# Optimization experiments

Measured on AMD Instinct MI355X. Metric: run time of the kernel, lower is better.

Reference implementation:

```python
import jax, jax.numpy as jnp
import numpy as np

NS = 33  # segments per image: id 0 = background, 1..32 = objects (fixed max-object count)
EPS_GN = 1e-5


def conv2d(x, w, b, pad):
    y = jax.lax.conv_general_dilated(x, w, window_strides=(1, 1),
                                     padding=[(pad, pad), (pad, pad)],
                                     dimension_numbers=('NCHW', 'OIHW', 'NCHW'))
    return y + b[None, :, None, None]


def group_norm(x, gamma, beta, groups):
    B, C, H, W = x.shape
    xg = x.reshape(B, groups, C // groups, H, W)
    mu = xg.mean((2, 3, 4), keepdims=True)
    var = xg.var((2, 3, 4), keepdims=True)
    xn = ((xg - mu) / jnp.sqrt(var + EPS_GN)).reshape(B, C, H, W)
    return xn * gamma[None, :, None, None] + beta[None, :, None, None]


def setup_inputs() -> dict:
    key = jax.random.key(0)
    ks = jax.random.split(key, 10)
    B, Cf, H, W = 4, 512, 128, 128
    std = 0.01
    inp = {
        'x': jax.random.normal(ks[0], (B, Cf, H, W), jnp.float32),
        'masks': jax.random.randint(ks[1], (B, H, W), 0, NS).astype(jnp.int32),
        # coord_conv: Conv2d(2, 64, 1)
        'w_coord': jax.random.normal(ks[2], (64, 2, 1, 1), jnp.float32) * std,
        'b_coord': jnp.zeros((64,), jnp.float32),
        # encoder convs + groupnorms
        'w1': jax.random.normal(ks[3], (256, Cf + 64, 3, 3), jnp.float32) * std,
        'b1': jnp.zeros((256,), jnp.float32),
        'g1': jnp.ones((256,), jnp.float32), 'bt1': jnp.zeros((256,), jnp.float32),
        'w2': jax.random.normal(ks[4], (128, 256, 3, 3), jnp.float32) * std,
        'b2': jnp.zeros((128,), jnp.float32),
        'g2': jnp.ones((128,), jnp.float32), 'bt2': jnp.zeros((128,), jnp.float32),
        'w3': jax.random.normal(ks[5], (64, 128, 3, 3), jnp.float32) * std,
        'b3': jnp.zeros((64,), jnp.float32),
        'g3': jnp.ones((64,), jnp.float32), 'bt3': jnp.zeros((64,), jnp.float32),
        # heads (1x1 convs on pooled [64] vectors == tiny matmuls)
        'w_box': jax.random.normal(ks[6], (7, 64, 1, 1), jnp.float32) * std,
        'b_box': jnp.zeros((7,), jnp.float32),
        'w_conf': jax.random.normal(ks[7], (1, 64, 1, 1), jnp.float32) * std,
        'b_conf': jnp.zeros((1,), jnp.float32),
    }
    return inp


def reference(x, masks, w_coord, b_coord, w1, b1, g1, bt1, w2, b2, g2, bt2,
              w3, b3, g3, bt3, w_box, b_box, w_conf, b_conf):
    B, _, H, W = x.shape
    # coordinate grid: channels are [grid_x, grid_y]
    gy, gx = jnp.meshgrid(jnp.arange(H), jnp.arange(W), indexing='ij')
    grid = jnp.stack([gx, gy], axis=0).astype(x.dtype)            # [2,H,W]
    grid = jnp.broadcast_to(grid[None], (B, 2, H, W))
    grid_feats = jax.nn.relu(conv2d(grid, w_coord, b_coord, 0))   # [B,64,H,W]

    h = jnp.concatenate([x, grid_feats], axis=1)                  # [B,576,H,W]
    h = jax.nn.relu(group_norm(conv2d(h, w1, b1, 1), g1, bt1, 8))
    h = jax.nn.relu(group_norm(conv2d(h, w2, b2, 1), g2, bt2, 4))
    h = jax.nn.relu(group_norm(conv2d(h, w3, b3, 1), g3, bt3, 4))  # [B,64,H,W]

    # per-(image, object-id) masked mean pooling via segment_sum
    C = h.shape[1]
    flat = h.transpose(0, 2, 3, 1).reshape(-1, C)                 # [B*H*W, 64]
    seg = (jnp.arange(B, dtype=jnp.int32)[:, None] * NS
           + masks.reshape(B, -1)).reshape(-1)                    # [B*H*W]
    sums = jax.ops.segment_sum(flat, seg, num_segments=B * NS).reshape(B, NS, C)
    counts = jax.ops.segment_sum(jnp.ones_like(seg, jnp.float32), seg,
                                 num_segments=B * NS).reshape(B, NS, 1)
    # drop background segment 0; safe divide matches the <1e-4 skip (empty slots -> 0 pooled)
    pooled = sums[:, 1:] / jnp.maximum(counts[:, 1:], 1e-4)       # [B,32,64]

    boxes = jnp.einsum('boc,kc->bok', pooled, w_box.reshape(7, C)) + b_box   # [B,32,7]
    scores = jnp.einsum('boc,c->bo', pooled, w_conf.reshape(C)) + b_conf[0]  # [B,32]
    return boxes, scores
```

## Files before the change

### kernel.cpp

```cpp
#include <hip/hip_runtime.h>

typedef unsigned short u16;
typedef unsigned int u32;
typedef __bf16 bf16x8 __attribute__((ext_vector_type(8)));
typedef float f32x4 __attribute__((ext_vector_type(4)));

__device__ __forceinline__ u16 f2bf(float f) {
  u32 u = __float_as_uint(f);
  u += 0x7fffu + ((u >> 16) & 1u);
  return (u16)(u >> 16);
}
__device__ __forceinline__ float bf2f(u16 h) {
  return __uint_as_float(((u32)h) << 16);
}

#define GLD_LDS16(g, l)                                                        \
  __builtin_amdgcn_global_load_lds(                                            \
      (__attribute__((address_space(1))) void*)(g),                            \
      (__attribute__((address_space(3))) void*)(l), 16, 0, 0)

__global__ __launch_bounds__(256) void init_k(float* smallb, u16* in1, u16* in2,
                                              u16* in3) {
  int bid = blockIdx.x;
  if (bid < 35) {
    int i = bid * 256 + threadIdx.x;
    if (i < 8708) smallb[i] = 0.f;
    return;
  }
  u16* buf;
  int C, sub;
  if (bid < 51)      { buf = in1; C = 576; sub = bid - 35; }
  else if (bid < 67) { buf = in2; C = 256; sub = bid - 51; }
  else               { buf = in3; C = 128; sub = bid - 67; }
  int b = sub >> 2, s = sub & 3;
  int npx = (s < 2) ? 130 : 128;
  u32* base = (u32*)(buf + (size_t)b * 130 * 130 * C);
  int C2 = C >> 1;
  int total = npx * C2;
  for (int i = threadIdx.x; i < total; i += 256) {
    int p = i / C2, r = i - p * C2;
    int y, x;
    if (s == 0)      { y = 0;     x = p; }
    else if (s == 1) { y = 129;   x = p; }
    else if (s == 2) { y = p + 1; x = 0; }
    else             { y = p + 1; x = 129; }
    base[(y * 130 + x) * C2 + r] = 0u;
  }
}

__global__ __launch_bounds__(256) void repack_all(const float* __restrict__ w1,
                                                  u16* __restrict__ wp1,
                                                  const float* __restrict__ w2,
                                                  u16* __restrict__ wp2,
                                                  const float* __restrict__ w3,
                                                  u16* __restrict__ wp3) {
  int bid = blockIdx.x;
  const float* src;
  u16* dst;
  int CIN, COUT, total, base;
  if (bid < 5184)      { src = w1; dst = wp1; CIN = 576; COUT = 256; total = 1327104; base = bid; }
  else if (bid < 6336) { src = w2; dst = wp2; CIN = 256; COUT = 128; total = 294912;  base = bid - 5184; }
  else                 { src = w3; dst = wp3; CIN = 128; COUT = 64;  total = 73728;   base = bid - 6336; }
  int idx = base * 256 + threadIdx.x;
  if (idx >= total) return;
  int kc = idx & 31;
  int n = (idx >> 5) % COUT;
  int q = idx / (32 * COUT);
  int dydx = q % 9, cb = q / 9;
  dst[idx] = f2bf(src[((size_t)n * CIN + cb * 32 + kc) * 9 + dydx]);
}

__global__ __launch_bounds__(256) void transpose_x(const float* __restrict__ x,
                                                   const float* __restrict__ wcd,
                                                   const float* __restrict__ bcd,
                                                   u16* __restrict__ in1) {
  const int bid = blockIdx.x;
  const int b = bid >> 8, h = (bid >> 1) & 127, half = bid & 1;
  const int w0 = half * 64;
  const int t = threadIdx.x;
  __shared__ u16 tile[128 * 65];
  __shared__ float swc[128], sbc[64];
  if (t < 128) swc[t] = wcd[t];
  else if (t < 192) sbc[t - 128] = bcd[t - 128];
  const int w = t & 63;
  const int cg = t >> 6;
  const float* xb = x + (((size_t)b * 512) * 128 + h) * 128 + w0 + w;
  u16* ob = in1 + ((size_t)(b * 130 + h + 1) * 130 + (w0 + 1)) * 576;
#pragma unroll 1
  for (int cc = 0; cc < 4; ++cc) {
    const int c0 = cc * 128;
#pragma unroll
    for (int j = 0; j < 32; ++j) {
      int cl = j * 4 + cg;
      tile[cl * 65 + w] = f2bf(xb[(size_t)(c0 + cl) * 16384]);
    }
    __syncthreads();
#pragma unroll
    for (int k = 0; k < 4; ++k) {
      int idx = k * 256 + t;
      int ww = idx >> 4, c8 = (idx & 15) * 8;
      union { uint4 u; u16 s[8]; } o;
#pragma unroll
      for (int i = 0; i < 8; ++i) o.s[i] = tile[(c8 + i) * 65 + ww];
      *(uint4*)(ob + (size_t)ww * 576 + c0 + c8) = o.u;
    }
    __syncthreads();
  }
  const int px = t >> 2, cq = (t & 3) * 16;
  const float fw = (float)(w0 + px), fh = (float)h;
  u16* gp = ob + (size_t)px * 576 + 512 + cq;
#pragma unroll
  for (int j = 0; j < 2; ++j) {
    union { uint4 u; u16 s[8]; } o;
#pragma unroll
    for (int i = 0; i < 8; ++i) {
      int c = cq + j * 8 + i;
      float v = swc[2 * c] * fw + swc[2 * c + 1] * fh + sbc[c];
      o.s[i] = f2bf(fmaxf(v, 0.f));
    }
    *(uint4*)(gp + j * 8) = o.u;
  }
}

template <int CIN, int COUT, int BN>
__global__ __launch_bounds__(256) void conv3x3_k(const u16* __restrict__ in,
                                                 const u16* __restrict__ wp,
                                                 const float* __restrict__ bias,
                                                 u16* __restrict__ out, int Hp,
                                                 int Wp, int opy, int opx,
                                                 float* __restrict__ stats,
                                                 int gsLog2, int nG) {
  constexpr int CB = CIN / 32;
  constexpr int WN = BN / 2;
  constexpr int NT = WN / 16;
  constexpr int ROWCH = 520;
  constexpr int NCH = 3 * ROWCH;
  constexpr int BUFE = 3 * 130 * 32;
  static_assert(BN == 128 || BN == 64, "");
  __shared__ u16 As3[2 * BUFE];
  __shared__ float redS[8], redQ[8];

  const int t = threadIdx.x;
  const int L = gridDim.x;
  const int work = (blockIdx.x & 7) * (L >> 3) + (blockIdx.x >> 3);
  const int xt = work >> 9;
  const int rem = work & 511;
  const int b = rem >> 7, h = rem & 127;
  const int n0 = xt * BN;

  const int lane = t & 63, wv = t >> 6;
  const int wm = wv & 1, wn = wv >> 1;
  const int ln = lane & 15, lq = lane >> 4;

  if (t < 8) { redS[t] = 0.f; redQ[t] = 0.f; }

  f32x4 acc[4][NT];
  const f32x4 zero = {0.f, 0.f, 0.f, 0.f};
#pragma unroll
  for (int i = 0; i < 4; ++i)
#pragma unroll
    for (int j = 0; j < NT; ++j) acc[i][j] = zero;

  const u16* inb = in + ((size_t)b * 130 + h) * 130 * CIN;

  int sc[7], srp[7], sqs[7];
#pragma unroll
  for (int it = 0; it < 7; ++it) {
    int c = it * 256 + t;
    sc[it] = (c < NCH) ? c : -1;
    int r = (c >= 2 * ROWCH) ? 2 : (c >= ROWCH ? 1 : 0);
    int wch = c - r * ROWCH;
    int pxi = wch >> 2, q = wch & 3;
    srp[it] = (r * 130 + pxi) * CIN + (q ^ ((pxi >> 1) & 3)) * 8;
    sqs[it] = c * 8;
  }

  auto stage = [&](int cb, int sel) {
    const u16* slab = inb + cb * 32;
    u16* dst = &As3[sel * BUFE];
#pragma unroll
    for (int it = 0; it < 7; ++it)
      if (sc[it] >= 0) GLD_LDS16(slab + srp[it], dst + sqs[it]);
  };

  stage(0, 0);

  const u16* wbase0 = wp + ((size_t)n0 + wn * WN + ln) * 32 + lq * 8;

#pragma unroll 1
  for (int cb = 0; cb < CB; ++cb) {
    __syncthreads();
    const int cur = cb & 1;
    if (cb + 1 < CB) stage(cb + 1, 1 - cur);
    const u16* wcb = wbase0 + (size_t)(cb * 9) * COUT * 32;
    const u16* As = &As3[cur * BUFE];

    bf16x8 fb[NT], fbn[NT];
#pragma unroll
    for (int j = 0; j < NT; ++j)
      fb[j] = *(const bf16x8*)(wcb + j * 512);
#pragma unroll
    for (int dydx = 0; dydx < 9; ++dydx) {
      const int dy = dydx / 3, dx = dydx % 3;
      if (dydx < 8) {
#pragma unroll
        for (int j = 0; j < NT; ++j)
          fbn[j] = *(const bf16x8*)(wcb + (size_t)(dydx + 1) * COUT * 32 + j * 512);
      }
      bf16x8 fa[4];
#pragma unroll
      for (int i = 0; i < 4; ++i) {
        int pxl = dx + wm * 64 + i * 16 + ln;
        int qs = lq ^ ((pxl >> 1) & 3);
        fa[i] = *(const bf16x8*)&As[((dy * 130 + pxl) << 5) + qs * 8];
      }
#pragma unroll
      for (int i = 0; i < 4; ++i)
#pragma unroll
        for (int j = 0; j < NT; ++j)
          acc[i][j] = __builtin_amdgcn_mfma_f32_16x16x32_bf16(fa[i], fb[j],
                                                              acc[i][j], 0, 0, 0);
#pragma unroll
      for (int j = 0; j < NT; ++j) fb[j] = fbn[j];
    }
  }

#pragma unroll
  for (int j = 0; j < NT; ++j) {
    const int n = n0 + wn * WN + j * 16 + ln;
    const float bv = bias[n];
    float sj = 0.f, qj = 0.f;
#pragma unroll
    for (int i = 0; i < 4; ++i) {
#pragma unroll
      for (int r = 0; r < 4; ++r) {
        const int w = wm * 64 + i * 16 + lq * 4 + r;
        u16 st = f2bf(acc[i][j][r] + bv);
        out[((size_t)(b * Hp + h + opy) * Wp + (w + opx)) * COUT + n] = st;
        float vq = bf2f(st);
        sj += vq;
        qj += vq * vq;
      }
    }
    sj += __shfl_xor(sj, 16, 64);
    sj += __shfl_xor(sj, 32, 64);
    qj += __shfl_xor(qj, 16, 64);
    qj += __shfl_xor(qj, 32, 64);
    if (lq == 0) {
      int gl = (wn * WN + j * 16 + ln) >> gsLog2;
      atomicAdd(&redS[gl], sj);
      atomicAdd(&redQ[gl], qj);
    }
  }
  __syncthreads();
  if (t < (BN >> gsLog2)) {
    int g = (n0 >> gsLog2) + t;
    atomicAdd(&stats[b * nG + g], redS[t]);
    atomicAdd(&stats[4 * nG + b * nG + g], redQ[t]);
  }
}

__global__ __launch_bounds__(256) void gn_norm(u16* __restrict__ buf,
                                               const float* __restrict__ stats,
                                               const float* __restrict__ gamma,
                                               const float* __restrict__ beta,
                                               int C, int gsLog2, int nG,
                                               float invCnt, int Hp, int Wp,
                                               int py, int px) {
  const int t = threadIdx.x;
  const int mt = blockIdx.x;
  const int b = mt >> 7, h = mt & 127;
  __shared__ float la[256], lb[256];
  for (int i = t; i < C; i += 256) {
    int g = i >> gsLog2;
    float mean = stats[b * nG + g] * invCnt;
    float m2 = stats[4 * nG + b * nG + g] * invCnt;
    float rstd = rsqrtf(m2 - mean * mean + 1e-5f);
    float a = gamma[i] * rstd;
    la[i] = a;
    lb[i] = beta[i] - mean * a;
  }
  __syncthreads();
  u16* row = buf + ((size_t)(b * Hp + h + py) * Wp + px) * C;
  const int n8 = 128 * C / 8;
  for (int v = t; v < n8; v += 256) {
    uint4 d = *(uint4*)(row + v * 8);
    int c0 = (v * 8) & (C - 1);
    u16* pp = (u16*)&d;
    union { uint4 u; u16 s[8]; } o;
#pragma unroll
    for (int i = 0; i < 8; ++i) {
      float xx = bf2f(pp[i]);
      float y = la[c0 + i] * xx + lb[c0 + i];
      o.s[i] = f2bf(fmaxf(y, 0.f));
    }
    *(uint4*)(row + v * 8) = o.u;
  }
}

__global__ __launch_bounds__(256) void pool_k(const u16* __restrict__ h3,
                                              const int* __restrict__ masks,
                                              const float* __restrict__ stats,
                                              const float* __restrict__ gamma,
                                              const float* __restrict__ beta,
                                              float* __restrict__ gsum,
                                              float* __restrict__ gcnt) {
  const int t = threadIdx.x;
  const int b = blockIdx.x >> 6, chunk = blockIdx.x & 63;
  __shared__ float ls[33 * 64];
  __shared__ float lc[33];
  for (int i = t; i < 33 * 64; i += 256) ls[i] = 0.f;
  if (t < 33) lc[t] = 0.f;
  const int c = t & 63;
  const int g = c >> 4;
  const float invCnt = 1.f / (16384.f * 16.f);
  float mean = stats[b * 4 + g] * invCnt;
  float m2 = stats[16 + b * 4 + g] * invCnt;
  float rstd = rsqrtf(m2 - mean * mean + 1e-5f);
  const float a = gamma[c] * rstd;
  const float cc = beta[c] - mean * a;
  __syncthreads();
  const int p0 = chunk * 256;
  for (int i = 0; i < 64; ++i) {
    int p = p0 + i * 4 + (t >> 6);
    int id = masks[b * 16384 + p];
    float v = bf2f(h3[((size_t)b * 16384 + p) * 64 + c]);
    v = fmaxf(a * v + cc, 0.f);
    atomicAdd(&ls[id * 64 + c], v);
    if (c == 0) atomicAdd(&lc[id], 1.f);
  }
  __syncthreads();
  for (int i = t; i < 33 * 64; i += 256) atomicAdd(&gsum[b * 2112 + i], ls[i]);
  if (t < 33) atomicAdd(&gcnt[b * 33 + t], lc[t]);
}

__global__ __launch_bounds__(256) void heads_k(const float* __restrict__ gsum,
                                               const float* __restrict__ gcnt,
                                               const float* __restrict__ wbox,
                                               const float* __restrict__ bbox,
                                               const float* __restrict__ wconf,
                                               const float* __restrict__ bconf,
                                               float* __restrict__ out) {
  int idx = blockIdx.x * 256 + threadIdx.x;
  if (idx >= 1024) return;
  if (idx < 896) {
    int b = idx / 224, r = idx % 224;
    int o = r / 7, k = r % 7;
    float inv = 1.f / fmaxf(gcnt[b * 33 + o + 1], 1e-4f);
    const float* ps = gsum + (b * 33 + o + 1) * 64;
    float s = 0.f;
    for (int c = 0; c < 64; ++c) s += ps[c] * wbox[k * 64 + c];
    out[idx] = s * inv + bbox[k];
  } else {
    int i = idx - 896;
    int b = i >> 5, o = i & 31;
    float inv = 1.f / fmaxf(gcnt[b * 33 + o + 1], 1e-4f);
    const float* ps = gsum + (b * 33 + o + 1) * 64;
    float s = 0.f;
    for (int c = 0; c < 64; ++c) s += ps[c] * wconf[c];
    out[896 + i] = s * inv + bconf[0];
  }
}

extern "C" void kernel_launch(void* const* d_in, const int* in_sizes, int n_in,
                              void* d_out, int out_size, void* d_ws,
                              size_t ws_size, hipStream_t stream) {
  (void)in_sizes; (void)n_in; (void)out_size; (void)ws_size;
  const float* x       = (const float*)d_in[0];
  const int*   masks   = (const int*)d_in[1];
  const float* w_coord = (const float*)d_in[2];
  const float* b_coord = (const float*)d_in[3];
  const float* w1  = (const float*)d_in[4];
  const float* b1  = (const float*)d_in[5];
  const float* g1  = (const float*)d_in[6];
  const float* bt1 = (const float*)d_in[7];
  const float* w2  = (const float*)d_in[8];
  const float* b2  = (const float*)d_in[9];
  const float* g2  = (const float*)d_in[10];
  const float* bt2 = (const float*)d_in[11];
  const float* w3  = (const float*)d_in[12];
  const float* b3  = (const float*)d_in[13];
  const float* g3  = (const float*)d_in[14];
  const float* bt3 = (const float*)d_in[15];
  const float* wbox  = (const float*)d_in[16];
  const float* bbox  = (const float*)d_in[17];
  const float* wconf = (const float*)d_in[18];
  const float* bconf = (const float*)d_in[19];
  float* out = (float*)d_out;

  char* ws = (char*)d_ws;
  size_t off = 0;
  auto take = [&](size_t bytes) {
    size_t o = off;
    off += (bytes + 255) & ~(size_t)255;
    return o;
  };
  u16* in1 = (u16*)(ws + take((size_t)4 * 130 * 130 * 576 * 2));
  u16* in2 = (u16*)(ws + take((size_t)4 * 130 * 130 * 256 * 2));
  u16* in3 = (u16*)(ws + take((size_t)4 * 130 * 130 * 128 * 2));
  u16* wp1 = (u16*)(ws + take((size_t)9 * 576 * 256 * 2));
  u16* wp2 = (u16*)(ws + take((size_t)9 * 256 * 128 * 2));
  u16* wp3 = (u16*)(ws + take((size_t)9 * 128 * 64 * 2));
  float* smallb = (float*)(ws + take(8708 * 4));
  u16* h3 = in1;

  float* s1   = smallb;
  float* s2   = smallb + 64;
  float* s3   = smallb + 96;
  float* psum = smallb + 128;
  float* pcnt = smallb + 8576;

  init_k<<<dim3(83), 256, 0, stream>>>(smallb, in1, in2, in3);

  repack_all<<<dim3(6624), 256, 0, stream>>>(w1, wp1, w2, wp2, w3, wp3);

  transpose_x<<<dim3(1024), 256, 0, stream>>>(x, w_coord, b_coord, in1);

  conv3x3_k<576, 256, 128><<<dim3(1024), 256, 0, stream>>>(in1, wp1, b1, in2, 130, 130, 1, 1, s1, 5, 8);
  gn_norm<<<dim3(512), 256, 0, stream>>>(in2, s1, g1, bt1, 256, 5, 8, 1.f / (16384.f * 32.f), 130, 130, 1, 1);

  conv3x3_k<256, 128, 128><<<dim3(512), 256, 0, stream>>>(in2, wp2, b2, in3, 130, 130, 1, 1, s2, 5, 4);
  gn_norm<<<dim3(512), 256, 0, stream>>>(in3, s2, g2, bt2, 128, 5, 4, 1.f / (16384.f * 32.f), 130, 130, 1, 1);

  conv3x3_k<128, 64, 64><<<dim3(512), 256, 0, stream>>>(in3, wp3, b3, h3, 128, 128, 0, 0, s3, 4, 4);

  pool_k<<<dim3(256), 256, 0, stream>>>(h3, masks, s3, g3, bt3, psum, pcnt);
  heads_k<<<dim3(4), 256, 0, stream>>>(psum, pcnt, wbox, bbox, wconf, bconf, out);
}
```

Before: 596.5 us.

## Fuse GroupNorm+ReLU into next conv's LDS staging and merge prep kernels

Removes the two standalone gn_norm passes by applying the previous layer's GroupNorm affine and ReLU to each input slab in LDS inside conv2 and conv3. Halo pixels are re-zeroed there so padding stays correct. The init, repack and transpose kernels are merged into one launch, and the A-fragment loads are software-pipelined one tap ahead. This saves two full read/write passes over the activations and several launches. In exchange it adds an extra barrier and per-element normalisation work in the conv inner loop, repeated for every output-column tile.

```diff
diff --git a/kernel.cpp b/kernel.cpp
--- a/kernel.cpp
+++ b/kernel.cpp
@@ -19,67 +19,64 @@
       (__attribute__((address_space(1))) void*)(g),                            \
       (__attribute__((address_space(3))) void*)(l), 16, 0, 0)
 
-__global__ __launch_bounds__(256) void init_k(float* smallb, u16* in1, u16* in2,
-                                              u16* in3) {
-  int bid = blockIdx.x;
-  if (bid < 35) {
-    int i = bid * 256 + threadIdx.x;
-    if (i < 8708) smallb[i] = 0.f;
-    return;
-  }
-  u16* buf;
-  int C, sub;
-  if (bid < 51)      { buf = in1; C = 576; sub = bid - 35; }
-  else if (bid < 67) { buf = in2; C = 256; sub = bid - 51; }
-  else               { buf = in3; C = 128; sub = bid - 67; }
-  int b = sub >> 2, s = sub & 3;
-  int npx = (s < 2) ? 130 : 128;
-  u32* base = (u32*)(buf + (size_t)b * 130 * 130 * C);
-  int C2 = C >> 1;
-  int total = npx * C2;
-  for (int i = threadIdx.x; i < total; i += 256) {
-    int p = i / C2, r = i - p * C2;
-    int y, x;
-    if (s == 0)      { y = 0;     x = p; }
-    else if (s == 1) { y = 129;   x = p; }
-    else if (s == 2) { y = p + 1; x = 0; }
-    else             { y = p + 1; x = 129; }
-    base[(y * 130 + x) * C2 + r] = 0u;
-  }
-}
-
-__global__ __launch_bounds__(256) void repack_all(const float* __restrict__ w1,
-                                                  u16* __restrict__ wp1,
-                                                  const float* __restrict__ w2,
-                                                  u16* __restrict__ wp2,
-                                                  const float* __restrict__ w3,
-                                                  u16* __restrict__ wp3) {
-  int bid = blockIdx.x;
-  const float* src;
-  u16* dst;
-  int CIN, COUT, total, base;
-  if (bid < 5184)      { src = w1; dst = wp1; CIN = 576; COUT = 256; total = 1327104; base = bid; }
-  else if (bid < 6336) { src = w2; dst = wp2; CIN = 256; COUT = 128; total = 294912;  base = bid - 5184; }
-  else                 { src = w3; dst = wp3; CIN = 128; COUT = 64;  total = 73728;   base = bid - 6336; }
-  int idx = base * 256 + threadIdx.x;
-  if (idx >= total) return;
-  int kc = idx & 31;
-  int n = (idx >> 5) % COUT;
-  int q = idx / (32 * COUT);
-  int dydx = q % 9, cb = q / 9;
-  dst[idx] = f2bf(src[((size_t)n * CIN + cb * 32 + kc) * 9 + dydx]);
-}
-
-__global__ __launch_bounds__(256) void transpose_x(const float* __restrict__ x,
-                                                   const float* __restrict__ wcd,
-                                                   const float* __restrict__ bcd,
-                                                   u16* __restrict__ in1) {
+__global__ __launch_bounds__(256) void prep_k(
+    float* smallb, u16* in1, u16* in2, u16* in3, const float* __restrict__ w1,
+    u16* __restrict__ wp1, const float* __restrict__ w2, u16* __restrict__ wp2,
+    const float* __restrict__ w3, u16* __restrict__ wp3,
+    const float* __restrict__ x, const float* __restrict__ wcd,
+    const float* __restrict__ bcd) {
   const int bid = blockIdx.x;
-  const int b = bid >> 8, h = (bid >> 1) & 127, half = bid & 1;
-  const int w0 = half * 64;
   const int t = threadIdx.x;
   __shared__ u16 tile[128 * 65];
   __shared__ float swc[128], sbc[64];
+
+  if (bid < 83) {
+    if (bid < 35) {
+      int i = bid * 256 + t;
+      if (i < 8708) smallb[i] = 0.f;
+      return;
+    }
+    u16* buf;
+    int C, sub;
+    if (bid < 51)      { buf = in1; C = 576; sub = bid - 35; }
+    else if (bid < 67) { buf = in2; C = 256; sub = bid - 51; }
+    else               { buf = in3; C = 128; sub = bid - 67; }
+    int b = sub >> 2, s = sub & 3;
+    int npx = (s < 2) ? 130 : 128;
+    u32* base = (u32*)(buf + (size_t)b * 130 * 130 * C);
+    int C2 = C >> 1;
+    int total = npx * C2;
+    for (int i = t; i < total; i += 256) {
+      int p = i / C2, r = i - p * C2;
+      int y, xx;
+      if (s == 0)      { y = 0;     xx = p; }
+      else if (s == 1) { y = 129;   xx = p; }
+      else if (s == 2) { y = p + 1; xx = 0; }
+      else             { y = p + 1; xx = 129; }
+      base[(y * 130 + xx) * C2 + r] = 0u;
+    }
+    return;
+  }
+  if (bid < 6707) {
+    int rel = bid - 83;
+    const float* src;
+    u16* dst;
+    int CIN, COUT, total, base;
+    if (rel < 5184)      { src = w1; dst = wp1; CIN = 576; COUT = 256; total = 1327104; base = rel; }
+    else if (rel < 6336) { src = w2; dst = wp2; CIN = 256; COUT = 128; total = 294912;  base = rel - 5184; }
+    else                 { src = w3; dst = wp3; CIN = 128; COUT = 64;  total = 73728;   base = rel - 6336; }
+    int idx = base * 256 + t;
+    if (idx >= total) return;
+    int kc = idx & 31;
+    int n = (idx >> 5) % COUT;
+    int q = idx / (32 * COUT);
+    int dydx = q % 9, cb = q / 9;
+    dst[idx] = f2bf(src[((size_t)n * CIN + cb * 32 + kc) * 9 + dydx]);
+    return;
+  }
+  const int tb = bid - 6707;
+  const int b = tb >> 8, h = (tb >> 1) & 127, half = tb & 1;
+  const int w0 = half * 64;
   if (t < 128) swc[t] = wcd[t];
   else if (t < 192) sbc[t - 128] = bcd[t - 128];
   const int w = t & 63;
@@ -122,14 +119,13 @@
   }
 }
 
-template <int CIN, int COUT, int BN>
-__global__ __launch_bounds__(256) void conv3x3_k(const u16* __restrict__ in,
-                                                 const u16* __restrict__ wp,
-                                                 const float* __restrict__ bias,
-                                                 u16* __restrict__ out, int Hp,
-                                                 int Wp, int opy, int opx,
-                                                 float* __restrict__ stats,
-                                                 int gsLog2, int nG) {
+template <int CIN, int COUT, int BN, bool NORM>
+__global__ __launch_bounds__(256) void conv3x3_k(
+    const u16* __restrict__ in, const u16* __restrict__ wp,
+    const float* __restrict__ bias, u16* __restrict__ out, int Hp, int Wp,
+    int opy, int opx, float* __restrict__ stats, int gsLog2, int nG,
+    const float* __restrict__ inStats, const float* __restrict__ inGamma,
+    const float* __restrict__ inBeta, int inGsLog2, int inNG) {
   constexpr int CB = CIN / 32;
   constexpr int WN = BN / 2;
   constexpr int NT = WN / 16;
@@ -139,6 +135,7 @@
   static_assert(BN == 128 || BN == 64, "");
   __shared__ u16 As3[2 * BUFE];
   __shared__ float redS[8], redQ[8];
+  __shared__ float la[NORM ? CIN : 1], lb[NORM ? CIN : 1];
 
   const int t = threadIdx.x;
   const int L = gridDim.x;
@@ -153,6 +150,18 @@
   const int ln = lane & 15, lq = lane >> 4;
 
   if (t < 8) { redS[t] = 0.f; redQ[t] = 0.f; }
+  if (NORM) {
+    const float invCnt = 1.f / (16384.f * 32.f);
+    for (int i = t; i < CIN; i += 256) {
+      int g = i >> inGsLog2;
+      float mean = inStats[b * inNG + g] * invCnt;
+      float m2 = inStats[4 * inNG + b * inNG + g] * invCnt;
+      float rstd = rsqrtf(m2 - mean * mean + 1e-5f);
+      float a = inGamma[i] * rstd;
+      la[i] = a;
+      lb[i] = inBeta[i] - mean * a;
+    }
+  }
 
   f32x4 acc[4][NT];
   const f32x4 zero = {0.f, 0.f, 0.f, 0.f};
@@ -163,7 +172,7 @@
 
   const u16* inb = in + ((size_t)b * 130 + h) * 130 * CIN;
 
-  int sc[7], srp[7], sqs[7];
+  int sc[7], srp[7], sqs[7], hz[7];
 #pragma unroll
   for (int it = 0; it < 7; ++it) {
     int c = it * 256 + t;
@@ -173,6 +182,8 @@
     int pxi = wch >> 2, q = wch & 3;
     srp[it] = (r * 130 + pxi) * CIN + (q ^ ((pxi >> 1) & 3)) * 8;
     sqs[it] = c * 8;
+    hz[it] = (pxi == 0) || (pxi == 129) || (r == 0 && h == 0) ||
+             (r == 2 && h == 127);
   }
 
   auto stage = [&](int cb, int sel) {
@@ -191,28 +202,57 @@
   for (int cb = 0; cb < CB; ++cb) {
     __syncthreads();
     const int cur = cb & 1;
+    const u16* wcb = wbase0 + (size_t)(cb * 9) * COUT * 32;
+    u16* Asw = &As3[cur * BUFE];
+
+    bf16x8 fb[NT], fbn[NT];
+#pragma unroll
+    for (int j = 0; j < NT; ++j) fb[j] = *(const bf16x8*)(wcb + j * 512);
+
+    if (NORM) {
+#pragma unroll
+      for (int it = 0; it < 7; ++it) {
+        if (sc[it] < 0) continue;
+        uint4* p = (uint4*)&Asw[sqs[it]];
+        if (hz[it]) {
+          *p = (uint4){0u, 0u, 0u, 0u};
+        } else {
+          int chb = cb * 32 + (srp[it] & 31);
+          union { uint4 u; u16 s[8]; } d;
+          d.u = *p;
+#pragma unroll
+          for (int e = 0; e < 8; ++e) {
+            float v = la[chb + e] * bf2f(d.s[e]) + lb[chb + e];
+            d.s[e] = f2bf(fmaxf(v, 0.f));
+          }
+          *p = d.u;
+        }
+      }
+      __syncthreads();
+    }
+
     if (cb + 1 < CB) stage(cb + 1, 1 - cur);
-    const u16* wcb = wbase0 + (size_t)(cb * 9) * COUT * 32;
-    const u16* As = &As3[cur * BUFE];
-
-    bf16x8 fb[NT], fbn[NT];
-#pragma unroll
-    for (int j = 0; j < NT; ++j)
-      fb[j] = *(const bf16x8*)(wcb + j * 512);
+
+    bf16x8 fa[4], fan[4];
+#pragma unroll
+    for (int i = 0; i < 4; ++i) {
+      int pxl = wm * 64 + i * 16 + ln;
+      int qs = lq ^ ((pxl >> 1) & 3);
+      fa[i] = *(const bf16x8*)&Asw[(pxl << 5) + qs * 8];
+    }
 #pragma unroll
     for (int dydx = 0; dydx < 9; ++dydx) {
-      const int dy = dydx / 3, dx = dydx % 3;
       if (dydx < 8) {
+        const int dyn = (dydx + 1) / 3, dxn = (dydx + 1) % 3;
 #pragma unroll
         for (int j = 0; j < NT; ++j)
           fbn[j] = *(const bf16x8*)(wcb + (size_t)(dydx + 1) * COUT * 32 + j * 512);
-      }
-      bf16x8 fa[4];
-#pragma unroll
-      for (int i = 0; i < 4; ++i) {
-        int pxl = dx + wm * 64 + i * 16 + ln;
-        int qs = lq ^ ((pxl >> 1) & 3);
-        fa[i] = *(const bf16x8*)&As[((dy * 130 + pxl) << 5) + qs * 8];
+#pragma unroll
+        for (int i = 0; i < 4; ++i) {
+          int pxl = dxn + wm * 64 + i * 16 + ln;
+          int qs = lq ^ ((pxl >> 1) & 3);
+          fan[i] = *(const bf16x8*)&Asw[((dyn * 130 + pxl) << 5) + qs * 8];
+        }
       }
 #pragma unroll
       for (int i = 0; i < 4; ++i)
@@ -222,6 +262,8 @@
                                                               acc[i][j], 0, 0, 0);
 #pragma unroll
       for (int j = 0; j < NT; ++j) fb[j] = fbn[j];
+#pragma unroll
+      for (int i = 0; i < 4; ++i) fa[i] = fan[i];
     }
   }
 
@@ -257,44 +299,6 @@
     int g = (n0 >> gsLog2) + t;
     atomicAdd(&stats[b * nG + g], redS[t]);
     atomicAdd(&stats[4 * nG + b * nG + g], redQ[t]);
-  }
-}
-
-__global__ __launch_bounds__(256) void gn_norm(u16* __restrict__ buf,
-                                               const float* __restrict__ stats,
-                                               const float* __restrict__ gamma,
-                                               const float* __restrict__ beta,
-                                               int C, int gsLog2, int nG,
-                                               float invCnt, int Hp, int Wp,
-                                               int py, int px) {
-  const int t = threadIdx.x;
-  const int mt = blockIdx.x;
-  const int b = mt >> 7, h = mt & 127;
-  __shared__ float la[256], lb[256];
-  for (int i = t; i < C; i += 256) {
-    int g = i >> gsLog2;
-    float mean = stats[b * nG + g] * invCnt;
-    float m2 = stats[4 * nG + b * nG + g] * invCnt;
-    float rstd = rsqrtf(m2 - mean * mean + 1e-5f);
-    float a = gamma[i] * rstd;
-    la[i] = a;
-    lb[i] = beta[i] - mean * a;
-  }
-  __syncthreads();
-  u16* row = buf + ((size_t)(b * Hp + h + py) * Wp + px) * C;
-  const int n8 = 128 * C / 8;
-  for (int v = t; v < n8; v += 256) {
-    uint4 d = *(uint4*)(row + v * 8);
-    int c0 = (v * 8) & (C - 1);
-    u16* pp = (u16*)&d;
-    union { uint4 u; u16 s[8]; } o;
-#pragma unroll
-    for (int i = 0; i < 8; ++i) {
-      float xx = bf2f(pp[i]);
-      float y = la[c0 + i] * xx + lb[c0 + i];
-      o.s[i] = f2bf(fmaxf(y, 0.f));
-    }
-    *(uint4*)(row + v * 8) = o.u;
   }
 }
 
@@ -410,19 +414,17 @@
   float* psum = smallb + 128;
   float* pcnt = smallb + 8576;
 
-  init_k<<<dim3(83), 256, 0, stream>>>(smallb, in1, in2, in3);
-
-  repack_all<<<dim3(6624), 256, 0, stream>>>(w1, wp1, w2, wp2, w3, wp3);
-
-  transpose_x<<<dim3(1024), 256, 0, stream>>>(x, w_coord, b_coord, in1);
-
-  conv3x3_k<576, 256, 128><<<dim3(1024), 256, 0, stream>>>(in1, wp1, b1, in2, 130, 130, 1, 1, s1, 5, 8);
-  gn_norm<<<dim3(512), 256, 0, stream>>>(in2, s1, g1, bt1, 256, 5, 8, 1.f / (16384.f * 32.f), 130, 130, 1, 1);
-
-  conv3x3_k<256, 128, 128><<<dim3(512), 256, 0, stream>>>(in2, wp2, b2, in3, 130, 130, 1, 1, s2, 5, 4);
-  gn_norm<<<dim3(512), 256, 0, stream>>>(in3, s2, g2, bt2, 128, 5, 4, 1.f / (16384.f * 32.f), 130, 130, 1, 1);
-
-  conv3x3_k<128, 64, 64><<<dim3(512), 256, 0, stream>>>(in3, wp3, b3, h3, 128, 128, 0, 0, s3, 4, 4);
+  prep_k<<<dim3(7731), 256, 0, stream>>>(smallb, in1, in2, in3, w1, wp1, w2,
+                                         wp2, w3, wp3, x, w_coord, b_coord);
+
+  conv3x3_k<576, 256, 128, false><<<dim3(1024), 256, 0, stream>>>(
+      in1, wp1, b1, in2, 130, 130, 1, 1, s1, 5, 8, nullptr, nullptr, nullptr, 0, 0);
+
+  conv3x3_k<256, 128, 128, true><<<dim3(512), 256, 0, stream>>>(
+      in2, wp2, b2, in3, 130, 130, 1, 1, s2, 5, 4, s1, g1, bt1, 5, 8);
+
+  conv3x3_k<128, 64, 64, true><<<dim3(512), 256, 0, stream>>>(
+      in3, wp3, b3, h3, 128, 128, 0, 0, s3, 4, 4, s2, g2, bt2, 5, 4);
 
   pool_k<<<dim3(256), 256, 0, stream>>>(h3, masks, s3, g3, bt3, psum, pcnt);
   heads_k<<<dim3(4), 256, 0, stream>>>(psum, pcnt, wbox, bbox, wconf, bconf, out);
```

Result: faster. 561.9 us (-5.8%).
